# Kernel optimization log

Measured on AMD Instinct MI355X. Metric: run time of the kernel, lower is better.

The kernel has to match this reference:

```python
import jax, jax.numpy as jnp
import numpy as np

LEVEL = 20            # module default -> 21 max-pool passes, kernels 1x1 .. 41x41 (H,W only)
K_SIG = 10.0          # init arg k: sigmoid weight sharpness
N_POOL = LEVEL + 1    # len(max_pool)
DENOM = N_POOL + 1    # torch: level = len(max_pool) + 1 = 22


def _edge3d(mask):
    # Equivalent to F.conv3d(mask, filt, padding=1) > 0 where filt is the
    # in-plane Laplacian: center 1, 4 H/W-neighbors -0.25, zeros elsewhere.
    p = jnp.pad(mask, ((0, 0), (0, 0), (0, 0), (1, 1), (1, 1)))
    lap = mask - 0.25 * (p[..., :-2, 1:-1] + p[..., 2:, 1:-1]
                         + p[..., 1:-1, :-2] + p[..., 1:-1, 2:])
    return (lap > 0).astype(jnp.float32)


def _mp3(x):
    # stride-1 3x3 max pool over H,W with same padding (pads with -inf like torch MaxPool)
    return jax.lax.reduce_window(x, -jnp.inf, jax.lax.max,
                                 (1, 1, 1, 3, 3), (1, 1, 1, 1, 1),
                                 ((0, 0), (0, 0), (0, 0), (1, 1), (1, 1)))


def _cal_dist(mask):
    edge = _edge3d(mask)  # [B,1,D,H,W] binary
    # maxpool with window (2k+1)x(2k+1) on a binary map == k cascaded 3x3 dilations,
    # so sum_{k=0}^{LEVEL} maxpool_{2k+1}(edge) is computed incrementally.
    def body(i, carry):
        e, acc = carry
        return (_mp3(e), acc + e)
    _, acc = jax.lax.fori_loop(0, N_POOL, body, (edge, jnp.zeros_like(edge)))
    return (DENOM - acc) / DENOM


def setup_inputs() -> dict:
    key = jax.random.key(0)
    k1, k2 = jax.random.split(key)
    outputs = jax.random.uniform(k1, (2, 1, 64, 256, 256), dtype=jnp.float32)
    masks = jax.random.randint(k2, (2, 1, 64, 256, 256), 0, 2, dtype=jnp.int32)
    return {"outputs": outputs, "masks": masks}


def reference(outputs, masks):
    eps = 1e-6
    m = masks.astype(jnp.float32)
    dist = _cal_dist(m)
    weight = jax.lax.stop_gradient(2.0 / (1.0 + jnp.exp(K_SIG * dist)))
    b = outputs.shape[0]
    ow = (outputs.astype(jnp.float32) * weight).reshape(b, -1)
    mw = (m * weight).reshape(b, -1)
    intersect = jnp.sum(ow * m.reshape(b, -1), axis=1)
    input_area = jnp.sum(ow, axis=1)
    target_area = jnp.sum(mw, axis=1)
    batch_loss = 1.0 - 2.0 * intersect / (input_area + target_area + 2.0 * eps)
    batch_loss = jnp.where(target_area == 0, 0.0, batch_loss)
    return batch_loss.mean()
```

## Files before the change

kernel.cpp:

```cpp
#include <hip/hip_runtime.h>
#include <stdint.h>

typedef unsigned long long u64;
typedef unsigned int u32;

#define HALO 21
#define BAND 64
#define MAXR (BAND + 2 * HALO)

__global__ __launch_bounds__(256) void bbsd_band(const float* __restrict__ outputs,
                                                 const int* __restrict__ masks,
                                                 float* __restrict__ acc,
                                                 u32* __restrict__ cnt,
                                                 float* __restrict__ out) {
    __shared__ u64 rows[MAXR][5];
    __shared__ u64 tmp[MAXR][5];
    __shared__ u64 pw[BAND][4][6];
    __shared__ float wtab[22];
    __shared__ float red[4][3];

    const int t = threadIdx.x;
    const int lane = t & 63, wv = t >> 6;
    const int slice = blockIdx.x >> 2;
    const int band = blockIdx.x & 3;
    const int b = slice >> 6;
    const int r0 = band * BAND;
    const int rs = (r0 - HALO < 0) ? 0 : r0 - HALO;
    const int re = (r0 + BAND + HALO > 256) ? 256 : r0 + BAND + HALO;
    const int R = re - rs;
    const int ioff = r0 - rs;

    if (t < 22) wtab[t] = 2.0f / (1.0f + __expf(10.0f * (float)(t + 1) * (1.0f / 22.0f)));

    {
        const int4* mp = (const int4*)(masks + (size_t)slice * 65536 + (size_t)rs * 256);
        const int total = R * 64;
        for (int idx = t; idx < total; idx += 256) {
            int4 v = mp[idx];
            u64 w = (u64)(v.x != 0) | ((u64)(v.y != 0) << 1)
                  | ((u64)(v.z != 0) << 2) | ((u64)(v.w != 0) << 3);
            w <<= (t & 15) * 4;
            w |= __shfl_down(w, 8, 16);
            w |= __shfl_down(w, 4, 16);
            w |= __shfl_down(w, 2, 16);
            w |= __shfl_down(w, 1, 16);
            if ((t & 15) == 0) {
                int widx = idx >> 4;
                rows[widx >> 2][widx & 3] = w;
            }
        }
    }
    __syncthreads();

    u64 m[4] = {0, 0, 0, 0}, c[4] = {0, 0, 0, 0};
    u64 p[5][4];
    #pragma unroll
    for (int pl = 0; pl < 5; ++pl)
        #pragma unroll
        for (int j = 0; j < 4; ++j) p[pl][j] = 0ull;

    if (t < R) {
        u64 up[4], dn[4];
        #pragma unroll
        for (int j = 0; j < 4; ++j) {
            m[j] = rows[t][j];
            up[j] = (t > 0)     ? rows[t - 1][j] : 0ull;
            dn[j] = (t < R - 1) ? rows[t + 1][j] : 0ull;
        }
        #pragma unroll
        for (int j = 0; j < 4; ++j) {
            u64 lf = (m[j] << 1) | (j > 0 ? (m[j - 1] >> 63) : 0ull);
            u64 rt = (m[j] >> 1) | (j < 3 ? (m[j + 1] << 63) : 0ull);
            c[j] = m[j] & ~(up[j] & dn[j] & lf & rt);
        }
    }

    for (int k = 1; k <= 20; ++k) {
        if (t < R) {
            #pragma unroll
            for (int j = 0; j < 4; ++j) {
                u64 lf = (c[j] << 1) | (j > 0 ? (c[j - 1] >> 63) : 0ull);
                u64 rt = (c[j] >> 1) | (j < 3 ? (c[j + 1] << 63) : 0ull);
                tmp[t][j] = c[j] | lf | rt;
            }
        }
        __syncthreads();
        int done = 1;
        if (t < R) {
            #pragma unroll
            for (int j = 0; j < 4; ++j) {
                u64 u_ = (t > 0)     ? tmp[t - 1][j] : 0ull;
                u64 d_ = (t < R - 1) ? tmp[t + 1][j] : 0ull;
                u64 n = tmp[t][j] | u_ | d_;
                u64 nw = n & ~c[j];
                c[j] = n;
                #pragma unroll
                for (int pl = 0; pl < 5; ++pl) {
                    u64 sel = (u64)0 - (u64)((k >> pl) & 1);
                    p[pl][j] |= nw & sel;
                }
            }
            done = ((c[0] & c[1] & c[2] & c[3]) == 0xFFFFFFFFFFFFFFFFull) ? 1 : 0;
        }
        if (__syncthreads_and(done)) break;
    }

    if (t >= ioff && t < ioff + BAND) {
        const int i = t - ioff;
        #pragma unroll
        for (int j = 0; j < 4; ++j) {
            u64 u_ = ~c[j];
            pw[i][j][0] = p[0][j] | u_;
            pw[i][j][1] = p[1][j];
            pw[i][j][2] = p[2][j] | u_;
            pw[i][j][3] = p[3][j];
            pw[i][j][4] = p[4][j] | u_;
            pw[i][j][5] = m[j];
        }
    }
    __syncthreads();

    float s0 = 0.0f, s1 = 0.0f, s2 = 0.0f;
    {
        const float4* op4 = (const float4*)outputs + (size_t)slice * 16384 + (size_t)r0 * 64;
        #pragma unroll
        for (int it = 0; it < 16; ++it) {
            int idx = it * 256 + t;
            float4 o4 = op4[idx];
            int rl = idx >> 6;
            int col = (idx * 4) & 255;
            int w = col >> 6, sh = col & 63;
            u64 P0 = pw[rl][w][0], P1 = pw[rl][w][1], P2 = pw[rl][w][2];
            u64 P3 = pw[rl][w][3], P4 = pw[rl][w][4], M = pw[rl][w][5];
            float ov[4] = {o4.x, o4.y, o4.z, o4.w};
            #pragma unroll
            for (int q = 0; q < 4; ++q) {
                int sq = sh + q;
                int d0 = (int)((P0 >> sq) & 1ull)
                       | ((int)((P1 >> sq) & 1ull) << 1)
                       | ((int)((P2 >> sq) & 1ull) << 2)
                       | ((int)((P3 >> sq) & 1ull) << 3)
                       | ((int)((P4 >> sq) & 1ull) << 4);
                float wgt = wtab[d0];
                float wm = ((M >> sq) & 1ull) ? wgt : 0.0f;
                s0 += ov[q] * wgt;
                s1 += wm;
                s2 += ov[q] * wm;
            }
        }
    }

    #pragma unroll
    for (int off = 32; off > 0; off >>= 1) {
        s0 += __shfl_down(s0, off);
        s1 += __shfl_down(s1, off);
        s2 += __shfl_down(s2, off);
    }
    if (lane == 0) { red[wv][0] = s0; red[wv][1] = s1; red[wv][2] = s2; }
    __syncthreads();
    if (t < 3) {
        float v = red[0][t] + red[1][t] + red[2][t] + red[3][t];
        atomicAdd(&acc[b * 3 + t], v);
        __threadfence();
    }
    __syncthreads();

    if (t == 0) {
        u32 old = __hip_atomic_fetch_add(cnt, 1u, __ATOMIC_ACQ_REL, __HIP_MEMORY_SCOPE_AGENT);
        if (old == 511u) {
            float s[6];
            #pragma unroll
            for (int k = 0; k < 6; ++k)
                s[k] = __hip_atomic_load(&acc[k], __ATOMIC_ACQUIRE, __HIP_MEMORY_SCOPE_AGENT);
            float loss = 0.0f;
            #pragma unroll
            for (int bb = 0; bb < 2; ++bb) {
                float A = s[bb * 3 + 0], T = s[bb * 3 + 1], I = s[bb * 3 + 2];
                loss += (T == 0.0f) ? 0.0f : (1.0f - 2.0f * I / (A + T + 2e-6f));
            }
            out[0] = 0.5f * loss;
        }
    }
}

extern "C" void kernel_launch(void* const* d_in, const int* in_sizes, int n_in,
                              void* d_out, int out_size, void* d_ws, size_t ws_size,
                              hipStream_t stream) {
    const float* outputs = (const float*)d_in[0];
    const int* masks = (const int*)d_in[1];
    float* out = (float*)d_out;
    float* acc = (float*)d_ws;
    u32* cnt = (u32*)((char*)d_ws + 24);

    hipMemsetAsync(d_ws, 0, 32, stream);
    bbsd_band<<<512, 256, 0, stream>>>(outputs, masks, acc, cnt, out);
}
```

Measured before the change: 129.0 us.

## Prefetch all mask and output tiles into registers up front with fixed band windows

Every band now processes a fixed 106-row window, so load trip counts are compile-time constants. Each thread issues all of its mask loads (27 int4) and output loads (16 float4) into registers before bit-packing and before the dilation loop, so global memory latency overlaps with the dilation work. The pw table is flattened to a 25-u64 row stride, likely to reduce LDS bank conflicts. The trade-off is high register pressure, which can cut occupancy or cause spills, and the edge bands now load extra rows.

```diff
diff --git a/kernel.cpp b/kernel.cpp
--- a/kernel.cpp
+++ b/kernel.cpp
@@ -6,16 +6,16 @@
 
 #define HALO 21
 #define BAND 64
-#define MAXR (BAND + 2 * HALO)
+#define RREG 106
 
 __global__ __launch_bounds__(256) void bbsd_band(const float* __restrict__ outputs,
                                                  const int* __restrict__ masks,
                                                  float* __restrict__ acc,
                                                  u32* __restrict__ cnt,
                                                  float* __restrict__ out) {
-    __shared__ u64 rows[MAXR][5];
-    __shared__ u64 tmp[MAXR][5];
-    __shared__ u64 pw[BAND][4][6];
+    __shared__ u64 rows[RREG][5];
+    __shared__ u64 tmp[RREG][5];
+    __shared__ u64 pw[BAND * 25];
     __shared__ float wtab[22];
     __shared__ float red[4][3];
 
@@ -25,29 +25,46 @@
     const int band = blockIdx.x & 3;
     const int b = slice >> 6;
     const int r0 = band * BAND;
-    const int rs = (r0 - HALO < 0) ? 0 : r0 - HALO;
-    const int re = (r0 + BAND + HALO > 256) ? 256 : r0 + BAND + HALO;
-    const int R = re - rs;
-    const int ioff = r0 - rs;
+    const int rs = (band == 0) ? 0 : (band == 3 ? 150 : r0 - HALO - (band == 2 ? 0 : 0));
+    const int rs2 = (band == 0) ? 0 : (band == 1) ? 43 : (band == 2) ? 107 : 150;
+    const int ioff = r0 - rs2;
+    (void)rs;
 
     if (t < 22) wtab[t] = 2.0f / (1.0f + __expf(10.0f * (float)(t + 1) * (1.0f / 22.0f)));
 
+    int4 mv[27];
     {
-        const int4* mp = (const int4*)(masks + (size_t)slice * 65536 + (size_t)rs * 256);
-        const int total = R * 64;
-        for (int idx = t; idx < total; idx += 256) {
-            int4 v = mp[idx];
-            u64 w = (u64)(v.x != 0) | ((u64)(v.y != 0) << 1)
-                  | ((u64)(v.z != 0) << 2) | ((u64)(v.w != 0) << 3);
-            w <<= (t & 15) * 4;
-            w |= __shfl_down(w, 8, 16);
-            w |= __shfl_down(w, 4, 16);
-            w |= __shfl_down(w, 2, 16);
-            w |= __shfl_down(w, 1, 16);
-            if ((t & 15) == 0) {
-                int widx = idx >> 4;
-                rows[widx >> 2][widx & 3] = w;
-            }
+        const int4* mp = (const int4*)(masks + (size_t)slice * 65536 + (size_t)rs2 * 256);
+        #pragma unroll
+        for (int i = 0; i < 27; ++i) {
+            int idx = i * 256 + t;
+            if (idx < RREG * 64) mv[i] = mp[idx];
+        }
+    }
+    float4 o[16];
+    {
+        const float4* op4 = (const float4*)outputs + (size_t)slice * 16384 + (size_t)r0 * 64;
+        #pragma unroll
+        for (int i = 0; i < 16; ++i) o[i] = op4[i * 256 + t];
+    }
+
+    #pragma unroll
+    for (int i = 0; i < 27; ++i) {
+        int idx = i * 256 + t;
+        u64 w = 0ull;
+        if (idx < RREG * 64) {
+            int4 v = mv[i];
+            w = (u64)(v.x != 0) | ((u64)(v.y != 0) << 1)
+              | ((u64)(v.z != 0) << 2) | ((u64)(v.w != 0) << 3);
+        }
+        w <<= (t & 15) * 4;
+        w |= __shfl_down(w, 8, 16);
+        w |= __shfl_down(w, 4, 16);
+        w |= __shfl_down(w, 2, 16);
+        w |= __shfl_down(w, 1, 16);
+        if (((t & 15) == 0) && idx < RREG * 64) {
+            int widx = idx >> 4;
+            rows[widx >> 2][widx & 3] = w;
         }
     }
     __syncthreads();
@@ -59,13 +76,13 @@
         #pragma unroll
         for (int j = 0; j < 4; ++j) p[pl][j] = 0ull;
 
-    if (t < R) {
+    if (t < RREG) {
         u64 up[4], dn[4];
         #pragma unroll
         for (int j = 0; j < 4; ++j) {
             m[j] = rows[t][j];
-            up[j] = (t > 0)     ? rows[t - 1][j] : 0ull;
-            dn[j] = (t < R - 1) ? rows[t + 1][j] : 0ull;
+            up[j] = (t > 0)        ? rows[t - 1][j] : 0ull;
+            dn[j] = (t < RREG - 1) ? rows[t + 1][j] : 0ull;
         }
         #pragma unroll
         for (int j = 0; j < 4; ++j) {
@@ -76,7 +93,7 @@
     }
 
     for (int k = 1; k <= 20; ++k) {
-        if (t < R) {
+        if (t < RREG) {
             #pragma unroll
             for (int j = 0; j < 4; ++j) {
                 u64 lf = (c[j] << 1) | (j > 0 ? (c[j - 1] >> 63) : 0ull);
@@ -86,11 +103,11 @@
         }
         __syncthreads();
         int done = 1;
-        if (t < R) {
+        if (t < RREG) {
             #pragma unroll
             for (int j = 0; j < 4; ++j) {
-                u64 u_ = (t > 0)     ? tmp[t - 1][j] : 0ull;
-                u64 d_ = (t < R - 1) ? tmp[t + 1][j] : 0ull;
+                u64 u_ = (t > 0)        ? tmp[t - 1][j] : 0ull;
+                u64 d_ = (t < RREG - 1) ? tmp[t + 1][j] : 0ull;
                 u64 n = tmp[t][j] | u_ | d_;
                 u64 nw = n & ~c[j];
                 c[j] = n;
@@ -110,43 +127,41 @@
         #pragma unroll
         for (int j = 0; j < 4; ++j) {
             u64 u_ = ~c[j];
-            pw[i][j][0] = p[0][j] | u_;
-            pw[i][j][1] = p[1][j];
-            pw[i][j][2] = p[2][j] | u_;
-            pw[i][j][3] = p[3][j];
-            pw[i][j][4] = p[4][j] | u_;
-            pw[i][j][5] = m[j];
+            const int base = i * 25 + j * 6;
+            pw[base + 0] = p[0][j] | u_;
+            pw[base + 1] = p[1][j];
+            pw[base + 2] = p[2][j] | u_;
+            pw[base + 3] = p[3][j];
+            pw[base + 4] = p[4][j] | u_;
+            pw[base + 5] = m[j];
         }
     }
     __syncthreads();
 
     float s0 = 0.0f, s1 = 0.0f, s2 = 0.0f;
-    {
-        const float4* op4 = (const float4*)outputs + (size_t)slice * 16384 + (size_t)r0 * 64;
-        #pragma unroll
-        for (int it = 0; it < 16; ++it) {
-            int idx = it * 256 + t;
-            float4 o4 = op4[idx];
-            int rl = idx >> 6;
-            int col = (idx * 4) & 255;
-            int w = col >> 6, sh = col & 63;
-            u64 P0 = pw[rl][w][0], P1 = pw[rl][w][1], P2 = pw[rl][w][2];
-            u64 P3 = pw[rl][w][3], P4 = pw[rl][w][4], M = pw[rl][w][5];
-            float ov[4] = {o4.x, o4.y, o4.z, o4.w};
-            #pragma unroll
-            for (int q = 0; q < 4; ++q) {
-                int sq = sh + q;
-                int d0 = (int)((P0 >> sq) & 1ull)
-                       | ((int)((P1 >> sq) & 1ull) << 1)
-                       | ((int)((P2 >> sq) & 1ull) << 2)
-                       | ((int)((P3 >> sq) & 1ull) << 3)
-                       | ((int)((P4 >> sq) & 1ull) << 4);
-                float wgt = wtab[d0];
-                float wm = ((M >> sq) & 1ull) ? wgt : 0.0f;
-                s0 += ov[q] * wgt;
-                s1 += wm;
-                s2 += ov[q] * wm;
-            }
+    #pragma unroll
+    for (int it = 0; it < 16; ++it) {
+        int idx = it * 256 + t;
+        int rl = idx >> 6;
+        int col = (idx << 2) & 255;
+        int w = col >> 6, sh = col & 63;
+        const int base = rl * 25 + w * 6;
+        u64 P0 = pw[base + 0], P1 = pw[base + 1], P2 = pw[base + 2];
+        u64 P3 = pw[base + 3], P4 = pw[base + 4], M = pw[base + 5];
+        float ov[4] = {o[it].x, o[it].y, o[it].z, o[it].w};
+        #pragma unroll
+        for (int q = 0; q < 4; ++q) {
+            int sq = sh + q;
+            int d0 = (int)((P0 >> sq) & 1ull)
+                   | ((int)((P1 >> sq) & 1ull) << 1)
+                   | ((int)((P2 >> sq) & 1ull) << 2)
+                   | ((int)((P3 >> sq) & 1ull) << 3)
+                   | ((int)((P4 >> sq) & 1ull) << 4);
+            float wgt = wtab[d0];
+            float wm = ((M >> sq) & 1ull) ? wgt : 0.0f;
+            s0 += ov[q] * wgt;
+            s1 += wm;
+            s2 += ov[q] * wm;
         }
     }
 
```

Result: faster. 116.5 us (-9.7%).
